# Kernel tuning notes

Hardware: AMD Instinct MI355X
Metric: run time of the kernel (lower is better)

Reference implementation:

```python
import math
import jax, jax.numpy as jnp
import numpy as np

EPS = 1.0
B, T, D, H = 8, 512, 768, 12
DH = D // H  # 64


def setup_inputs() -> dict:
    key = jax.random.key(0)
    ks = jax.random.split(key, 10)
    std = 0.02
    return {
        "x": jax.random.normal(ks[0], (B, T, D), dtype=jnp.float32),
        "r_position_embedding": jax.random.normal(ks[1], (T, D), dtype=jnp.float32),
        "r_content_bias": jax.random.normal(ks[2], (H, DH), dtype=jnp.float32),
        "r_position_bias": jax.random.normal(ks[3], (H, DH), dtype=jnp.float32),
        # Conv1D(linear) params, stored as (in, out) so y = x @ W + b
        "Wqkv": jax.random.normal(ks[4], (D, 3 * D), dtype=jnp.float32) * std,
        "bqkv": jnp.zeros((3 * D,), dtype=jnp.float32),
        "Wh": jax.random.normal(ks[5], (D, D), dtype=jnp.float32) * std,
        "bh": jnp.zeros((D,), dtype=jnp.float32),
        "Wp": jax.random.normal(ks[6], (D, D), dtype=jnp.float32) * std,
        "bp": jnp.zeros((D,), dtype=jnp.float32),
    }


def reference(x, r_position_embedding, r_content_bias, r_position_bias,
              Wqkv, bqkv, Wh, bh, Wp, bp):
    # QKV projection and head split
    qkv = x @ Wqkv + bqkv                                   # (B,T,3D)
    q, k, v = jnp.split(qkv, 3, axis=-1)
    split_heads = lambda t: t.reshape(B, T, H, DH).transpose(0, 2, 1, 3)  # (B,H,T,DH)
    q, k, v = split_heads(q), split_heads(k), split_heads(v)

    # content scores
    scores = jnp.einsum('bhtd,bhsd->bhts', q, k)            # (B,H,T,T)

    # relative position projection: linear is row-wise, so project once then gather.
    # rel_pos[c, r] = linear_position(pos_emb[max(0, c - r)])
    proj = (r_position_embedding @ Wp + bp).reshape(T, H, DH)  # (P=T, H, DH)
    idx = jnp.maximum(0, jnp.arange(T)[:, None] - jnp.arange(T)[None, :])  # (T,T) = max(0, c-r)

    # q . rel_pos term: compute vs all P distinct positions, then gather per (c, r)
    rel_q = jnp.einsum('bhtd,phd->bhtp', q, proj)           # (B,H,T,P)
    scores = scores + jnp.take_along_axis(rel_q, idx[None, None, :, :], axis=-1)

    # content-bias and position-bias terms (query-independent)
    bias_c = jnp.einsum('hd,phd->hp', r_content_bias, proj)[:, idx]   # (H,T,T)
    bias_p = jnp.einsum('hd,phd->hp', r_position_bias, proj)[:, idx]  # (H,T,T)
    scores = scores + bias_c[None] + bias_p[None]

    # masked softmax with EPS=1 quirks (faithful to original)
    scores = scores / (math.sqrt(DH) + EPS)
    mask = jnp.tril(jnp.ones((T, T), dtype=jnp.float32))    # causal
    masked_exps = jnp.exp(scores) * mask
    att = masked_exps / (masked_exps.sum(-1, keepdims=True) + 2.0 * EPS)

    ctx = jnp.einsum('bhts,bhsd->bhtd', att, v)             # (B,H,T,DH)
    # original: permute(0,2,3,1) then flatten -> (B,T,DH*H) interleaving (d, h)
    ctx = ctx.transpose(0, 2, 3, 1).reshape(B, T, D)
    out = ctx @ Wh + bh
    k_out = k.transpose(0, 1, 3, 2)                         # (B,H,DH,T) as module returns
    return out, k_out, v
```

## Files before the change

### kernel.cpp

```cpp
#include <hip/hip_runtime.h>
#include <hip/hip_bf16.h>


#define NT 512
#define ND 768
#define NH 12

typedef short short4_t __attribute__((ext_vector_type(4)));
typedef short short8_t __attribute__((ext_vector_type(8)));
typedef float float4_t __attribute__((ext_vector_type(4)));

__device__ __forceinline__ float b2f(unsigned short u) {
    union { unsigned int i; float f; } x; x.i = ((unsigned int)u) << 16; return x.f;
}
__device__ __forceinline__ unsigned short f2b(float f) {
    union { float f; unsigned int i; } x; x.f = f;
    unsigned int i = x.i;
    i += 0x7fffu + ((i >> 16) & 1u);
    return (unsigned short)(i >> 16);
}

__global__ __launch_bounds__(256) void prep(
    const float* __restrict__ x, unsigned short* __restrict__ xb,
    const float* __restrict__ rpe, unsigned short* __restrict__ rpeb,
    const float* __restrict__ Wqkv, unsigned short* __restrict__ WqkvT,
    const float* __restrict__ Wh, unsigned short* __restrict__ WhT,
    const float* __restrict__ Wp, unsigned short* __restrict__ WpT)
{
    __shared__ float t[32][33];
    const int bid = blockIdx.x;
    const int tid = threadIdx.x;

    if (bid < 1728) {
        const bool isx = bid < 1536;
        const float* in = isx ? x : rpe;
        unsigned short* out = isx ? xb : rpeb;
        const int i = (isx ? bid : bid - 1536) * 256 + tid;
        const float* s = in + (size_t)i * 8;
        float4_t f0 = *(const float4_t*)s;
        float4_t f1 = *(const float4_t*)(s + 4);
        union { short8_t v; unsigned short u[8]; } pk;
        pk.u[0] = f2b(f0[0]); pk.u[1] = f2b(f0[1]); pk.u[2] = f2b(f0[2]); pk.u[3] = f2b(f0[3]);
        pk.u[4] = f2b(f1[0]); pk.u[5] = f2b(f1[1]); pk.u[6] = f2b(f1[2]); pk.u[7] = f2b(f1[3]);
        *(short8_t*)&out[(size_t)i * 8] = pk.v;
        return;
    }
    const float* in; unsigned short* out; int K, N, k0, n0;
    if (bid < 3456) {
        const int tt = bid - 1728;
        in = Wqkv; out = WqkvT; K = 768; N = 2304;
        n0 = (tt % 72) * 32; k0 = (tt / 72) * 32;
    } else if (bid < 4032) {
        const int tt = bid - 3456;
        in = Wh; out = WhT; K = 768; N = 768;
        n0 = (tt % 24) * 32; k0 = (tt / 24) * 32;
    } else {
        const int tt = bid - 4032;
        in = Wp; out = WpT; K = 768; N = 768;
        n0 = (tt % 24) * 32; k0 = (tt / 24) * 32;
    }
    const int r = tid >> 3;
    const int c = (tid & 7) * 4;
    float4_t v = *(const float4_t*)&in[(size_t)(k0 + r) * N + n0 + c];
    t[r][c + 0] = v[0]; t[r][c + 1] = v[1]; t[r][c + 2] = v[2]; t[r][c + 3] = v[3];
    __syncthreads();
    union { short4_t v; unsigned short u[4]; } pk;
    pk.u[0] = f2b(t[c + 0][r]);
    pk.u[1] = f2b(t[c + 1][r]);
    pk.u[2] = f2b(t[c + 2][r]);
    pk.u[3] = f2b(t[c + 3][r]);
    *(short4_t*)&out[(size_t)(n0 + r) * K + k0 + c] = pk.v;
}

__global__ __launch_bounds__(256) void gemm_qkv(
    const unsigned short* __restrict__ A, const unsigned short* __restrict__ BT,
    const float* __restrict__ biasf,
    unsigned short* __restrict__ ob0, float* __restrict__ o1, float* __restrict__ o2,
    unsigned short* __restrict__ sh1, unsigned short* __restrict__ sh2,
    const unsigned short* __restrict__ Ap, const unsigned short* __restrict__ BTp,
    const float* __restrict__ biasp, const float* __restrict__ rcb,
    const float* __restrict__ rpb, unsigned short* __restrict__ projb,
    float* __restrict__ biascp)
{
    __shared__ __attribute__((aligned(16))) unsigned short Al[3][128 * 32];
    __shared__ __attribute__((aligned(16))) unsigned short Bl[3][128 * 32];

    const int K    = 768;
    const int tid  = threadIdx.x;
    const int bid  = blockIdx.x;
    const int wave = tid >> 6;
    const int lane = tid & 63;
    const int lm   = lane & 15;
    const int quad = lane >> 4;
    const int wr   = (wave >> 1) * 64;
    const int wc   = (wave & 1) * 64;

    int m0, n0; bool proj;
    const unsigned short *Asrc, *Bsrc;
    if (bid >= 24) {
        int qb = bid - 24;
        qb = (qb & 7) * 72 + (qb >> 3);
        m0 = (qb / 18) * 128; n0 = (qb % 18) * 128;
        Asrc = A; Bsrc = BT; proj = false;
    } else {
        m0 = (bid / 6) * 128; n0 = (bid % 6) * 128;
        Asrc = Ap; Bsrc = BTp; proj = true;
    }

    float4_t acc[4][4];
#pragma unroll
    for (int mt = 0; mt < 4; ++mt)
#pragma unroll
        for (int nt = 0; nt < 4; ++nt)
#pragma unroll
            for (int r = 0; r < 4; ++r) acc[mt][nt][r] = 0.f;

    const unsigned short* ap = Asrc + (size_t)(m0 + (tid >> 2)) * K + (tid & 3) * 8;
    const unsigned short* bp = Bsrc + (size_t)(n0 + (tid >> 2)) * K + (tid & 3) * 8;
    const size_t rstep = (size_t)64 * K;

    auto stage = [&](int bi, int k0) {
        unsigned short* al0 = &Al[bi][0] + wave * 512;
        unsigned short* bl0 = &Bl[bi][0] + wave * 512;
        __builtin_amdgcn_global_load_lds(
            (const __attribute__((address_space(1))) void*)(ap + k0),
            (__attribute__((address_space(3))) void*)al0, 16, 0, 0);
        __builtin_amdgcn_global_load_lds(
            (const __attribute__((address_space(1))) void*)(ap + rstep + k0),
            (__attribute__((address_space(3))) void*)(al0 + 2048), 16, 0, 0);
        __builtin_amdgcn_global_load_lds(
            (const __attribute__((address_space(1))) void*)(bp + k0),
            (__attribute__((address_space(3))) void*)bl0, 16, 0, 0);
        __builtin_amdgcn_global_load_lds(
            (const __attribute__((address_space(1))) void*)(bp + rstep + k0),
            (__attribute__((address_space(3))) void*)(bl0 + 2048), 16, 0, 0);
    };

    stage(0, 0);
    stage(1, 32);

    int cur = 0;
    for (int k0 = 0; k0 < K; k0 += 32) {
        if (k0 + 32 < K) asm volatile("s_waitcnt vmcnt(4)" ::: "memory");
        else             asm volatile("s_waitcnt vmcnt(0)" ::: "memory");
        __builtin_amdgcn_s_barrier();
        __builtin_amdgcn_sched_barrier(0);

        if (k0 + 64 < K) stage((cur + 2) % 3, k0 + 64);

        short8_t af[4], bf[4];
#pragma unroll
        for (int mt = 0; mt < 4; ++mt)
            af[mt] = *(const short8_t*)&Al[cur][(wr + mt * 16 + lm) * 32 + quad * 8];
#pragma unroll
        for (int nt = 0; nt < 4; ++nt)
            bf[nt] = *(const short8_t*)&Bl[cur][(wc + nt * 16 + lm) * 32 + quad * 8];
#pragma unroll
        for (int mt = 0; mt < 4; ++mt)
#pragma unroll
            for (int nt = 0; nt < 4; ++nt)
                acc[mt][nt] = __builtin_amdgcn_mfma_f32_16x16x32_bf16(af[mt], bf[nt], acc[mt][nt], 0, 0, 0);

        cur = (cur + 1) % 3;
    }

    if (!proj) {
        const int sec = n0 / 768;
#pragma unroll
        for (int nt = 0; nt < 4; ++nt) {
            const int gcol = n0 + wc + nt * 16 + lm;
            const int cc = gcol - sec * 768;
            const int h = cc >> 6, d = cc & 63;
            const float bv = biasf[gcol];
#pragma unroll
            for (int mt = 0; mt < 4; ++mt)
#pragma unroll
                for (int r = 0; r < 4; ++r) {
                    const int grow = m0 + wr + mt * 16 + quad * 4 + r;
                    const int b = grow >> 9, t = grow & 511;
                    const float val = acc[mt][nt][r] + bv;
                    if (sec == 0) {
                        ob0[((size_t)((b * NH + h) * NT + t)) * 64 + d] = f2b(val);
                    } else if (sec == 1) {
                        o1[((size_t)((b * NH + h) * 64 + d)) * NT + t] = val;
                        sh1[((size_t)((b * NH + h) * NT + t)) * 64 + d] = f2b(val);
                    } else {
                        o2[((size_t)((b * NH + h) * NT + t)) * 64 + d] = val;
                        sh2[((size_t)((b * NH + h) * 64 + d)) * NT + t] = f2b(val);
                    }
                }
        }
    } else {
        const int h = (n0 + wc) >> 6;
        float part[4][4];
#pragma unroll
        for (int mt = 0; mt < 4; ++mt)
#pragma unroll
            for (int r = 0; r < 4; ++r) part[mt][r] = 0.f;
#pragma unroll
        for (int nt = 0; nt < 4; ++nt) {
            const int gcol = n0 + wc + nt * 16 + lm;
            const int d = nt * 16 + lm;
            const float bv = biasp[gcol];
            const float cb = rcb[h * 64 + d] + rpb[h * 64 + d];
#pragma unroll
            for (int mt = 0; mt < 4; ++mt)
#pragma unroll
                for (int r = 0; r < 4; ++r) {
                    const int grow = m0 + wr + mt * 16 + quad * 4 + r;
                    const float val = acc[mt][nt][r] + bv;
                    projb[((size_t)(h * NT + grow)) * 64 + d] = f2b(val);
                    part[mt][r] += val * cb;
                }
        }
#pragma unroll
        for (int mt = 0; mt < 4; ++mt)
#pragma unroll
            for (int r = 0; r < 4; ++r) {
                float v = part[mt][r];
                v += __shfl_xor(v, 1); v += __shfl_xor(v, 2);
                v += __shfl_xor(v, 4); v += __shfl_xor(v, 8);
                if (lm == 0)
                    biascp[h * NT + m0 + wr + mt * 16 + quad * 4 + r] = v;
            }
    }
}

__global__ __launch_bounds__(256) void gemm_out(
    const unsigned short* __restrict__ A, const unsigned short* __restrict__ BT,
    const float* __restrict__ biasf, float* __restrict__ o1)
{
    __shared__ __attribute__((aligned(16))) unsigned short Al[3][64 * 32];
    __shared__ __attribute__((aligned(16))) unsigned short Bl[3][128 * 32];

    const int K    = 768;
    const int tid  = threadIdx.x;
    const int bid  = (blockIdx.x & 7) * 48 + (blockIdx.x >> 3);
    const int wave = tid >> 6;
    const int lane = tid & 63;
    const int lm   = lane & 15;
    const int quad = lane >> 4;
    const int wr   = (wave >> 1) * 32;
    const int wc   = (wave & 1) * 64;

    const int m0 = (bid / 6) * 64;
    const int n0 = (bid % 6) * 128;

    float4_t acc[2][4];
#pragma unroll
    for (int mt = 0; mt < 2; ++mt)
#pragma unroll
        for (int nt = 0; nt < 4; ++nt)
#pragma unroll
            for (int r = 0; r < 4; ++r) acc[mt][nt][r] = 0.f;

    const unsigned short* ap = A  + (size_t)(m0 + (tid >> 2)) * K + (tid & 3) * 8;
    const unsigned short* bp = BT + (size_t)(n0 + (tid >> 2)) * K + (tid & 3) * 8;
    const size_t rstep = (size_t)64 * K;

    auto stage = [&](int bi, int k0) {
        unsigned short* al0 = &Al[bi][0] + wave * 512;
        unsigned short* bl0 = &Bl[bi][0] + wave * 512;
        __builtin_amdgcn_global_load_lds(
            (const __attribute__((address_space(1))) void*)(ap + k0),
            (__attribute__((address_space(3))) void*)al0, 16, 0, 0);
        __builtin_amdgcn_global_load_lds(
            (const __attribute__((address_space(1))) void*)(bp + k0),
            (__attribute__((address_space(3))) void*)bl0, 16, 0, 0);
        __builtin_amdgcn_global_load_lds(
            (const __attribute__((address_space(1))) void*)(bp + rstep + k0),
            (__attribute__((address_space(3))) void*)(bl0 + 2048), 16, 0, 0);
    };

    stage(0, 0);
    stage(1, 32);

    int cur = 0;
    for (int k0 = 0; k0 < K; k0 += 32) {
        if (k0 + 32 < K) asm volatile("s_waitcnt vmcnt(3)" ::: "memory");
        else             asm volatile("s_waitcnt vmcnt(0)" ::: "memory");
        __builtin_amdgcn_s_barrier();
        __builtin_amdgcn_sched_barrier(0);

        if (k0 + 64 < K) stage((cur + 2) % 3, k0 + 64);

        short8_t af[2], bf[4];
#pragma unroll
        for (int mt = 0; mt < 2; ++mt)
            af[mt] = *(const short8_t*)&Al[cur][(wr + mt * 16 + lm) * 32 + quad * 8];
#pragma unroll
        for (int nt = 0; nt < 4; ++nt)
            bf[nt] = *(const short8_t*)&Bl[cur][(wc + nt * 16 + lm) * 32 + quad * 8];
#pragma unroll
        for (int mt = 0; mt < 2; ++mt)
#pragma unroll
            for (int nt = 0; nt < 4; ++nt)
                acc[mt][nt] = __builtin_amdgcn_mfma_f32_16x16x32_bf16(af[mt], bf[nt], acc[mt][nt], 0, 0, 0);

        cur = (cur + 1) % 3;
    }

#pragma unroll
    for (int nt = 0; nt < 4; ++nt) {
        const int gcol = n0 + wc + nt * 16 + lm;
        const float bv = biasf[gcol];
#pragma unroll
        for (int mt = 0; mt < 2; ++mt)
#pragma unroll
            for (int r = 0; r < 4; ++r) {
                const int grow = m0 + wr + mt * 16 + quad * 4 + r;
                o1[(size_t)grow * ND + gcol] = acc[mt][nt][r] + bv;
            }
    }
}

__global__ __launch_bounds__(128) void attn_mfma(
    const unsigned short* __restrict__ q_ws, const unsigned short* __restrict__ k_ws,
    const unsigned short* __restrict__ v_ws, const unsigned short* __restrict__ projb,
    const float* __restrict__ biascp, unsigned short* __restrict__ ctxT)
{
    __shared__ unsigned short Kt[64][72];
    __shared__ unsigned short Vt[64][72];
    __shared__ unsigned short pP[96][72];
    __shared__ float          Rl[2][16][84];
    __shared__ unsigned short esl[2][16][72];

    const int tid   = threadIdx.x;
    const int y     = blockIdx.y;
    const int h     = y % NH;
    const int b     = y / NH;
    const int pairi = blockIdx.x;
    const int wave  = tid >> 6;
    const int lane  = tid & 63;
    const int lm    = lane & 15;
    const int quad  = lane >> 4;
    const int koff  = quad * 8;

    const int sr = tid >> 1;
    const int sc = (tid & 1) * 32;

    for (int c = 0; c < 2; ++c) {
        const int ti  = c ? pairi : (15 - pairi);
        const int tb0 = ti * 32;
        const int tw0 = tb0 + wave * 16;
        const int nst = (tb0 >> 6) + 1;

        short8_t aq[2];
        aq[0] = *(const short8_t*)&q_ws[((size_t)(y * NT + tw0 + lm)) * 64 + koff];
        aq[1] = *(const short8_t*)&q_ws[((size_t)(y * NT + tw0 + lm)) * 64 + koff + 32];

        float4_t ctxacc[4];
#pragma unroll
        for (int j = 0; j < 4; ++j)
#pragma unroll
            for (int r = 0; r < 4; ++r) ctxacc[j][r] = 0.f;
        float esum[4] = {0.f, 0.f, 0.f, 0.f};

        for (int st = 0; st < nst; ++st) {
            const int s0      = st * 64;
            const int plo_blk = max(0, tb0 - s0 - 63);
            const int cnt_blk = tb0 + 31 - s0 - plo_blk + 1;
            if (c | st) __syncthreads();
            {
                const unsigned short* ks = &k_ws[((size_t)(y * NT + s0 + sr)) * 64 + sc];
                *(short8_t*)&Kt[sr][sc]      = *(const short8_t*)ks;
                *(short8_t*)&Kt[sr][sc + 8]  = *(const short8_t*)(ks + 8);
                *(short8_t*)&Kt[sr][sc + 16] = *(const short8_t*)(ks + 16);
                *(short8_t*)&Kt[sr][sc + 24] = *(const short8_t*)(ks + 24);
                const unsigned short* vs = &v_ws[((size_t)(y * 64 + sr)) * NT + s0 + sc];
                *(short8_t*)&Vt[sr][sc]      = *(const short8_t*)vs;
                *(short8_t*)&Vt[sr][sc + 8]  = *(const short8_t*)(vs + 8);
                *(short8_t*)&Vt[sr][sc + 16] = *(const short8_t*)(vs + 16);
                *(short8_t*)&Vt[sr][sc + 24] = *(const short8_t*)(vs + 24);
                for (int p = tid; p < cnt_blk; p += 128) {
                    const unsigned short* ps = &projb[((size_t)(h * NT + plo_blk + p)) * 64];
                    *(short8_t*)&pP[p][0]  = *(const short8_t*)ps;
                    *(short8_t*)&pP[p][8]  = *(const short8_t*)(ps + 8);
                    *(short8_t*)&pP[p][16] = *(const short8_t*)(ps + 16);
                    *(short8_t*)&pP[p][24] = *(const short8_t*)(ps + 24);
                    *(short8_t*)&pP[p][32] = *(const short8_t*)(ps + 32);
                    *(short8_t*)&pP[p][40] = *(const short8_t*)(ps + 40);
                    *(short8_t*)&pP[p][48] = *(const short8_t*)(ps + 48);
                    *(short8_t*)&pP[p][56] = *(const short8_t*)(ps + 56);
                }
            }
            __syncthreads();

            if (s0 <= tw0 + 15) {
                const int plo_w = max(0, tw0 - s0 - 63);
                const int pbase = plo_w - plo_blk;
                const int cntw  = tw0 + 15 - s0 - plo_w + 1;
                const int jmax  = min(3, (tw0 + 15 - s0) >> 4);
                const int jpmax = (cntw - 1) >> 4;

                float4_t accQK[4];
#pragma unroll
                for (int j = 0; j < 4; ++j)
#pragma unroll
                    for (int r = 0; r < 4; ++r) accQK[j][r] = 0.f;
                for (int j = 0; j <= jmax; ++j) {
                    short8_t bk0 = *(const short8_t*)&Kt[j * 16 + lm][koff];
                    short8_t bk1 = *(const short8_t*)&Kt[j * 16 + lm][koff + 32];
                    accQK[j] = __builtin_amdgcn_mfma_f32_16x16x32_bf16(aq[0], bk0, accQK[j], 0, 0, 0);
                    accQK[j] = __builtin_amdgcn_mfma_f32_16x16x32_bf16(aq[1], bk1, accQK[j], 0, 0, 0);
                }
                for (int j = 0; j <= jpmax; ++j) {
                    short8_t bp0 = *(const short8_t*)&pP[pbase + j * 16 + lm][koff];
                    short8_t bp1 = *(const short8_t*)&pP[pbase + j * 16 + lm][koff + 32];
                    float4_t accR;
#pragma unroll
                    for (int r = 0; r < 4; ++r) accR[r] = 0.f;
                    accR = __builtin_amdgcn_mfma_f32_16x16x32_bf16(aq[0], bp0, accR, 0, 0, 0);
                    accR = __builtin_amdgcn_mfma_f32_16x16x32_bf16(aq[1], bp1, accR, 0, 0, 0);
                    const int p = j * 16 + lm;
                    const float bv = biascp[h * NT + min(plo_w + p, NT - 1)];
#pragma unroll
                    for (int r = 0; r < 4; ++r) Rl[wave][quad * 4 + r][p] = accR[r] + bv;
                }
                asm volatile("" ::: "memory");

#pragma unroll
                for (int j = 0; j < 4; ++j) {
                    const int s_g = s0 + j * 16 + lm;
#pragma unroll
                    for (int r = 0; r < 4; ++r) {
                        const int t_g = tw0 + quad * 4 + r;
                        float e = 0.f;
                        if (s_g <= t_g) {
                            const int p = t_g - s_g - plo_w;
                            e = __expf(fminf((accQK[j][r] + Rl[wave][quad * 4 + r][p]) * (1.f / 9.f), 60.f));
                        }
                        esl[wave][quad * 4 + r][j * 16 + lm] = f2b(e);
                        esum[r] += e;
                    }
                }
                asm volatile("" ::: "memory");

                short8_t ae0 = *(const short8_t*)&esl[wave][lm][koff];
                short8_t ae1 = *(const short8_t*)&esl[wave][lm][koff + 32];
#pragma unroll
                for (int j = 0; j < 4; ++j) {
                    short8_t bv0 = *(const short8_t*)&Vt[j * 16 + lm][koff];
                    short8_t bv1 = *(const short8_t*)&Vt[j * 16 + lm][koff + 32];
                    ctxacc[j] = __builtin_amdgcn_mfma_f32_16x16x32_bf16(ae0, bv0, ctxacc[j], 0, 0, 0);
                    ctxacc[j] = __builtin_amdgcn_mfma_f32_16x16x32_bf16(ae1, bv1, ctxacc[j], 0, 0, 0);
                }
            }
        }

        float rcpv[4];
#pragma unroll
        for (int r = 0; r < 4; ++r) {
            float v = esum[r];
            v += __shfl_xor(v, 1); v += __shfl_xor(v, 2);
            v += __shfl_xor(v, 4); v += __shfl_xor(v, 8);
            rcpv[r] = 1.f / (v + 2.f);
        }
#pragma unroll
        for (int j = 0; j < 4; ++j) {
            const int d = j * 16 + lm;
#pragma unroll
            for (int r = 0; r < 4; ++r) {
                const int t = tw0 + quad * 4 + r;
                ctxT[((size_t)(b * NT + t)) * ND + d * NH + h] = f2b(ctxacc[j][r] * rcpv[r]);
            }
        }
    }
}

extern "C" void kernel_launch(void* const* d_in, const int* in_sizes, int n_in,
                              void* d_out, int out_size, void* d_ws, size_t ws_size,
                              hipStream_t stream)
{
    const float* x    = (const float*)d_in[0];
    const float* rpe  = (const float*)d_in[1];
    const float* rcb  = (const float*)d_in[2];
    const float* rpb  = (const float*)d_in[3];
    const float* Wqkv = (const float*)d_in[4];
    const float* bqkv = (const float*)d_in[5];
    const float* Wh   = (const float*)d_in[6];
    const float* bh   = (const float*)d_in[7];
    const float* Wp   = (const float*)d_in[8];
    const float* bp   = (const float*)d_in[9];

    float* out  = (float*)d_out;
    float* kout = out + 3145728;
    float* vout = out + 6291456;

    unsigned short* q_ws  = (unsigned short*)d_ws;
    unsigned short* k_ws  = q_ws + 3145728;
    unsigned short* v_ws  = k_ws + 3145728;
    unsigned short* ctxT  = v_ws + 3145728;
    unsigned short* xb    = ctxT;
    unsigned short* projb = ctxT + 3145728;
    float* biascp = (float*)(projb + 393216);
    unsigned short* WqkvT = (unsigned short*)(biascp + 6144);
    unsigned short* WhT   = WqkvT + 1769472;
    unsigned short* rpeb  = (unsigned short*)out;
    unsigned short* WpT   = rpeb + 393216;

    prep<<<dim3(4608), 256, 0, stream>>>(x, xb, rpe, rpeb, Wqkv, WqkvT, Wh, WhT, Wp, WpT);

    gemm_qkv<<<dim3(600), 256, 0, stream>>>(
        xb, WqkvT, bqkv, q_ws, kout, vout, k_ws, v_ws,
        rpeb, WpT, bp, rcb, rpb, projb, biascp);
    attn_mfma<<<dim3(8, 96), 128, 0, stream>>>(
        q_ws, k_ws, v_ws, projb, biascp, ctxT);
    gemm_out<<<dim3(384), 256, 0, stream>>>(
        ctxT, WhT, bh, out);
}
```

Measured before the change: 208.3 us.

## Split projection GEMM into its own kernel, drop triple-buffering, remap attention blocks per XCD

The fused QKV/projection GEMM is split into two kernels, gemm_projL with 24 blocks and gemm_qkv with 576. Both now use a single LDS buffer with two __syncthreads per k-step instead of the three-stage async global_load_lds pipeline. The attention launch changes from a 2D grid to a 1D grid whose block index is remapped so each XCD gets 12 consecutive (batch, head) pairs, aiming for better L2 locality. Dropping the multi-stage pipeline lowers LDS use and may raise occupancy, but it exposes memory latency each k-step and adds one kernel launch.

```diff
diff --git a/kernel.cpp b/kernel.cpp
--- a/kernel.cpp
+++ b/kernel.cpp
@@ -72,22 +72,20 @@
     *(short4_t*)&out[(size_t)(n0 + r) * K + k0 + c] = pk.v;
 }
 
-__global__ __launch_bounds__(256) void gemm_qkv(
+__global__ __launch_bounds__(256) void gemm_projL(
     const unsigned short* __restrict__ A, const unsigned short* __restrict__ BT,
-    const float* __restrict__ biasf,
-    unsigned short* __restrict__ ob0, float* __restrict__ o1, float* __restrict__ o2,
-    unsigned short* __restrict__ sh1, unsigned short* __restrict__ sh2,
-    const unsigned short* __restrict__ Ap, const unsigned short* __restrict__ BTp,
     const float* __restrict__ biasp, const float* __restrict__ rcb,
     const float* __restrict__ rpb, unsigned short* __restrict__ projb,
     float* __restrict__ biascp)
 {
-    __shared__ __attribute__((aligned(16))) unsigned short Al[3][128 * 32];
-    __shared__ __attribute__((aligned(16))) unsigned short Bl[3][128 * 32];
+    __shared__ __attribute__((aligned(16))) unsigned short Al[128 * 32];
+    __shared__ __attribute__((aligned(16))) unsigned short Bl[128 * 32];
 
     const int K    = 768;
     const int tid  = threadIdx.x;
     const int bid  = blockIdx.x;
+    const int m0   = (bid / 6) * 128;
+    const int n0   = (bid % 6) * 128;
     const int wave = tid >> 6;
     const int lane = tid & 63;
     const int lm   = lane & 15;
@@ -95,18 +93,6 @@
     const int wr   = (wave >> 1) * 64;
     const int wc   = (wave & 1) * 64;
 
-    int m0, n0; bool proj;
-    const unsigned short *Asrc, *Bsrc;
-    if (bid >= 24) {
-        int qb = bid - 24;
-        qb = (qb & 7) * 72 + (qb >> 3);
-        m0 = (qb / 18) * 128; n0 = (qb % 18) * 128;
-        Asrc = A; Bsrc = BT; proj = false;
-    } else {
-        m0 = (bid / 6) * 128; n0 = (bid % 6) * 128;
-        Asrc = Ap; Bsrc = BTp; proj = true;
-    }
-
     float4_t acc[4][4];
 #pragma unroll
     for (int mt = 0; mt < 4; ++mt)
@@ -115,13 +101,14 @@
 #pragma unroll
             for (int r = 0; r < 4; ++r) acc[mt][nt][r] = 0.f;
 
-    const unsigned short* ap = Asrc + (size_t)(m0 + (tid >> 2)) * K + (tid & 3) * 8;
-    const unsigned short* bp = Bsrc + (size_t)(n0 + (tid >> 2)) * K + (tid & 3) * 8;
+    const unsigned short* ap = A  + (size_t)(m0 + (tid >> 2)) * K + (tid & 3) * 8;
+    const unsigned short* bp = BT + (size_t)(n0 + (tid >> 2)) * K + (tid & 3) * 8;
     const size_t rstep = (size_t)64 * K;
-
-    auto stage = [&](int bi, int k0) {
-        unsigned short* al0 = &Al[bi][0] + wave * 512;
-        unsigned short* bl0 = &Bl[bi][0] + wave * 512;
+    unsigned short* al0 = Al + wave * 512;
+    unsigned short* bl0 = Bl + wave * 512;
+
+    for (int k0 = 0; k0 < K; k0 += 32) {
+        if (k0) __syncthreads();
         __builtin_amdgcn_global_load_lds(
             (const __attribute__((address_space(1))) void*)(ap + k0),
             (__attribute__((address_space(3))) void*)al0, 16, 0, 0);
@@ -134,95 +121,147 @@
         __builtin_amdgcn_global_load_lds(
             (const __attribute__((address_space(1))) void*)(bp + rstep + k0),
             (__attribute__((address_space(3))) void*)(bl0 + 2048), 16, 0, 0);
-    };
-
-    stage(0, 0);
-    stage(1, 32);
-
-    int cur = 0;
-    for (int k0 = 0; k0 < K; k0 += 32) {
-        if (k0 + 32 < K) asm volatile("s_waitcnt vmcnt(4)" ::: "memory");
-        else             asm volatile("s_waitcnt vmcnt(0)" ::: "memory");
-        __builtin_amdgcn_s_barrier();
-        __builtin_amdgcn_sched_barrier(0);
-
-        if (k0 + 64 < K) stage((cur + 2) % 3, k0 + 64);
+        __syncthreads();
 
         short8_t af[4], bf[4];
 #pragma unroll
         for (int mt = 0; mt < 4; ++mt)
-            af[mt] = *(const short8_t*)&Al[cur][(wr + mt * 16 + lm) * 32 + quad * 8];
+            af[mt] = *(const short8_t*)&Al[(wr + mt * 16 + lm) * 32 + quad * 8];
 #pragma unroll
         for (int nt = 0; nt < 4; ++nt)
-            bf[nt] = *(const short8_t*)&Bl[cur][(wc + nt * 16 + lm) * 32 + quad * 8];
+            bf[nt] = *(const short8_t*)&Bl[(wc + nt * 16 + lm) * 32 + quad * 8];
 #pragma unroll
         for (int mt = 0; mt < 4; ++mt)
 #pragma unroll
             for (int nt = 0; nt < 4; ++nt)
                 acc[mt][nt] = __builtin_amdgcn_mfma_f32_16x16x32_bf16(af[mt], bf[nt], acc[mt][nt], 0, 0, 0);
-
-        cur = (cur + 1) % 3;
-    }
-
-    if (!proj) {
-        const int sec = n0 / 768;
-#pragma unroll
-        for (int nt = 0; nt < 4; ++nt) {
-            const int gcol = n0 + wc + nt * 16 + lm;
-            const int cc = gcol - sec * 768;
-            const int h = cc >> 6, d = cc & 63;
-            const float bv = biasf[gcol];
-#pragma unroll
-            for (int mt = 0; mt < 4; ++mt)
-#pragma unroll
-                for (int r = 0; r < 4; ++r) {
-                    const int grow = m0 + wr + mt * 16 + quad * 4 + r;
-                    const int b = grow >> 9, t = grow & 511;
-                    const float val = acc[mt][nt][r] + bv;
-                    if (sec == 0) {
-                        ob0[((size_t)((b * NH + h) * NT + t)) * 64 + d] = f2b(val);
-                    } else if (sec == 1) {
-                        o1[((size_t)((b * NH + h) * 64 + d)) * NT + t] = val;
-                        sh1[((size_t)((b * NH + h) * NT + t)) * 64 + d] = f2b(val);
-                    } else {
-                        o2[((size_t)((b * NH + h) * NT + t)) * 64 + d] = val;
-                        sh2[((size_t)((b * NH + h) * 64 + d)) * NT + t] = f2b(val);
-                    }
+    }
+
+    const int h = (n0 + wc) >> 6;
+    float part[4][4];
+#pragma unroll
+    for (int mt = 0; mt < 4; ++mt)
+#pragma unroll
+        for (int r = 0; r < 4; ++r) part[mt][r] = 0.f;
+#pragma unroll
+    for (int nt = 0; nt < 4; ++nt) {
+        const int gcol = n0 + wc + nt * 16 + lm;
+        const int d = nt * 16 + lm;
+        const float bv = biasp[gcol];
+        const float cb = rcb[h * 64 + d] + rpb[h * 64 + d];
+#pragma unroll
+        for (int mt = 0; mt < 4; ++mt)
+#pragma unroll
+            for (int r = 0; r < 4; ++r) {
+                const int grow = m0 + wr + mt * 16 + quad * 4 + r;
+                const float val = acc[mt][nt][r] + bv;
+                projb[((size_t)(h * NT + grow)) * 64 + d] = f2b(val);
+                part[mt][r] += val * cb;
+            }
+    }
+#pragma unroll
+    for (int mt = 0; mt < 4; ++mt)
+#pragma unroll
+        for (int r = 0; r < 4; ++r) {
+            float v = part[mt][r];
+            v += __shfl_xor(v, 1); v += __shfl_xor(v, 2);
+            v += __shfl_xor(v, 4); v += __shfl_xor(v, 8);
+            if (lm == 0)
+                biascp[h * NT + m0 + wr + mt * 16 + quad * 4 + r] = v;
+        }
+}
+
+__global__ __launch_bounds__(256) void gemm_qkv(
+    const unsigned short* __restrict__ A, const unsigned short* __restrict__ BT,
+    const float* __restrict__ biasf,
+    unsigned short* __restrict__ ob0, float* __restrict__ o1, float* __restrict__ o2,
+    unsigned short* __restrict__ sh1, unsigned short* __restrict__ sh2)
+{
+    __shared__ __attribute__((aligned(16))) unsigned short Al[128 * 32];
+    __shared__ __attribute__((aligned(16))) unsigned short Bl[128 * 32];
+
+    const int K    = 768;
+    const int tid  = threadIdx.x;
+    int qb = blockIdx.x;
+    qb = (qb & 7) * 72 + (qb >> 3);
+    const int m0   = (qb / 18) * 128;
+    const int n0   = (qb % 18) * 128;
+    const int wave = tid >> 6;
+    const int lane = tid & 63;
+    const int lm   = lane & 15;
+    const int quad = lane >> 4;
+    const int wr   = (wave >> 1) * 64;
+    const int wc   = (wave & 1) * 64;
+
+    float4_t acc[4][4];
+#pragma unroll
+    for (int mt = 0; mt < 4; ++mt)
+#pragma unroll
+        for (int nt = 0; nt < 4; ++nt)
+#pragma unroll
+            for (int r = 0; r < 4; ++r) acc[mt][nt][r] = 0.f;
+
+    const unsigned short* ap = A  + (size_t)(m0 + (tid >> 2)) * K + (tid & 3) * 8;
+    const unsigned short* bp = BT + (size_t)(n0 + (tid >> 2)) * K + (tid & 3) * 8;
+    const size_t rstep = (size_t)64 * K;
+    unsigned short* al0 = Al + wave * 512;
+    unsigned short* bl0 = Bl + wave * 512;
+
+    for (int k0 = 0; k0 < K; k0 += 32) {
+        if (k0) __syncthreads();
+        __builtin_amdgcn_global_load_lds(
+            (const __attribute__((address_space(1))) void*)(ap + k0),
+            (__attribute__((address_space(3))) void*)al0, 16, 0, 0);
+        __builtin_amdgcn_global_load_lds(
+            (const __attribute__((address_space(1))) void*)(ap + rstep + k0),
+            (__attribute__((address_space(3))) void*)(al0 + 2048), 16, 0, 0);
+        __builtin_amdgcn_global_load_lds(
+            (const __attribute__((address_space(1))) void*)(bp + k0),
+            (__attribute__((address_space(3))) void*)bl0, 16, 0, 0);
+        __builtin_amdgcn_global_load_lds(
+            (const __attribute__((address_space(1))) void*)(bp + rstep + k0),
+            (__attribute__((address_space(3))) void*)(bl0 + 2048), 16, 0, 0);
+        __syncthreads();
+
+        short8_t af[4], bf[4];
+#pragma unroll
+        for (int mt = 0; mt < 4; ++mt)
+            af[mt] = *(const short8_t*)&Al[(wr + mt * 16 + lm) * 32 + quad * 8];
+#pragma unroll
+        for (int nt = 0; nt < 4; ++nt)
+            bf[nt] = *(const short8_t*)&Bl[(wc + nt * 16 + lm) * 32 + quad * 8];
+#pragma unroll
+        for (int mt = 0; mt < 4; ++mt)
+#pragma unroll
+            for (int nt = 0; nt < 4; ++nt)
+                acc[mt][nt] = __builtin_amdgcn_mfma_f32_16x16x32_bf16(af[mt], bf[nt], acc[mt][nt], 0, 0, 0);
+    }
+
+    const int sec = n0 / 768;
+#pragma unroll
+    for (int nt = 0; nt < 4; ++nt) {
+        const int gcol = n0 + wc + nt * 16 + lm;
+        const int cc = gcol - sec * 768;
+        const int h = cc >> 6, d = cc & 63;
+        const float bv = biasf[gcol];
+#pragma unroll
+        for (int mt = 0; mt < 4; ++mt) {
+#pragma unroll
+            for (int r = 0; r < 4; ++r) {
+                const int grow = m0 + wr + mt * 16 + quad * 4 + r;
+                const int b = grow >> 9, t = grow & 511;
+                const float val = acc[mt][nt][r] + bv;
+                if (sec == 0) {
+                    ob0[((size_t)((b * NH + h) * NT + t)) * 64 + d] = f2b(val);
+                } else if (sec == 1) {
+                    o1[((size_t)((b * NH + h) * 64 + d)) * NT + t] = val;
+                    sh1[((size_t)((b * NH + h) * NT + t)) * 64 + d] = f2b(val);
+                } else {
+                    o2[((size_t)((b * NH + h) * NT + t)) * 64 + d] = val;
+                    sh2[((size_t)((b * NH + h) * 64 + d)) * NT + t] = f2b(val);
                 }
+            }
         }
-    } else {
-        const int h = (n0 + wc) >> 6;
-        float part[4][4];
-#pragma unroll
-        for (int mt = 0; mt < 4; ++mt)
-#pragma unroll
-            for (int r = 0; r < 4; ++r) part[mt][r] = 0.f;
-#pragma unroll
-        for (int nt = 0; nt < 4; ++nt) {
-            const int gcol = n0 + wc + nt * 16 + lm;
-            const int d = nt * 16 + lm;
-            const float bv = biasp[gcol];
-            const float cb = rcb[h * 64 + d] + rpb[h * 64 + d];
-#pragma unroll
-            for (int mt = 0; mt < 4; ++mt)
-#pragma unroll
-                for (int r = 0; r < 4; ++r) {
-                    const int grow = m0 + wr + mt * 16 + quad * 4 + r;
-                    const float val = acc[mt][nt][r] + bv;
-                    projb[((size_t)(h * NT + grow)) * 64 + d] = f2b(val);
-                    part[mt][r] += val * cb;
-                }
-        }
-#pragma unroll
-        for (int mt = 0; mt < 4; ++mt)
-#pragma unroll
-            for (int r = 0; r < 4; ++r) {
-                float v = part[mt][r];
-                v += __shfl_xor(v, 1); v += __shfl_xor(v, 2);
-                v += __shfl_xor(v, 4); v += __shfl_xor(v, 8);
-                if (lm == 0)
-                    biascp[h * NT + m0 + wr + mt * 16 + quad * 4 + r] = v;
-            }
     }
 }
 
@@ -326,10 +365,13 @@
     __shared__ unsigned short esl[2][16][72];
 
     const int tid   = threadIdx.x;
-    const int y     = blockIdx.y;
+    const int bid   = blockIdx.x;
+    const int xcd   = bid & 7;
+    const int jj    = bid >> 3;
+    const int y     = xcd * 12 + (jj >> 3);
+    const int pairi = jj & 7;
     const int h     = y % NH;
     const int b     = y / NH;
-    const int pairi = blockIdx.x;
     const int wave  = tid >> 6;
     const int lane  = tid & 63;
     const int lm    = lane & 15;
@@ -501,10 +543,11 @@
 
     prep<<<dim3(4608), 256, 0, stream>>>(x, xb, rpe, rpeb, Wqkv, WqkvT, Wh, WhT, Wp, WpT);
 
-    gemm_qkv<<<dim3(600), 256, 0, stream>>>(
-        xb, WqkvT, bqkv, q_ws, kout, vout, k_ws, v_ws,
+    gemm_projL<<<dim3(24), 256, 0, stream>>>(
         rpeb, WpT, bp, rcb, rpb, projb, biascp);
-    attn_mfma<<<dim3(8, 96), 128, 0, stream>>>(
+    gemm_qkv<<<dim3(576), 256, 0, stream>>>(
+        xb, WqkvT, bqkv, q_ws, kout, vout, k_ws, v_ws);
+    attn_mfma<<<dim3(768), 128, 0, stream>>>(
         q_ws, k_ws, v_ws, projb, biascp, ctxT);
     gemm_out<<<dim3(384), 256, 0, stream>>>(
         ctxT, WhT, bh, out);
```

Result: no change. 206.2 us (-1.0%).
